# Kernel optimization log

Hardware: AMD Instinct MI355X
Metric: run time of the kernel (lower is better)

Reference implementation:

```python
import jax, jax.numpy as jnp
import numpy as np

N_NODES = 100000
N_EDGES = 1600000
N_GRAPHS = 1024


def gcn_conv(x, src, dst, W, b, num_nodes):
    # GCNConv: x' = D^{-1/2} (A + I) D^{-1/2} x W + b  (self-loops already appended to src/dst)
    h = x @ W  # [N, out]
    deg = jax.ops.segment_sum(jnp.ones_like(dst, dtype=h.dtype), dst, num_segments=num_nodes)
    dinv = jnp.where(deg > 0, jax.lax.rsqrt(jnp.maximum(deg, 1.0)), 0.0)
    norm = dinv[src] * dinv[dst]  # [E]
    msg = h[src] * norm[:, None]  # [E, out]  <- dominant memory traffic
    return jax.ops.segment_sum(msg, dst, num_segments=num_nodes) + b


def global_mean_pool(x, batch, num_graphs):
    s = jax.ops.segment_sum(x, batch, num_segments=num_graphs)
    cnt = jax.ops.segment_sum(jnp.ones((x.shape[0],), x.dtype), batch, num_segments=num_graphs)
    return s / jnp.maximum(cnt, 1.0)[:, None]


def setup_inputs() -> dict:
    key = jax.random.key(0)
    ks = jax.random.split(key, 12)
    x = jax.random.normal(ks[0], (N_NODES, 4), dtype=jnp.float32)
    edge_index = jax.random.randint(ks[1], (2, N_EDGES), 0, N_NODES, dtype=jnp.int64)
    batch = jnp.sort(jax.random.randint(ks[2], (N_NODES,), 0, N_GRAPHS, dtype=jnp.int64))
    def glorot(k, shape):
        fan = shape[0] + shape[1]
        return jax.random.normal(k, shape, jnp.float32) * jnp.sqrt(2.0 / fan)
    return {
        "x": x, "edge_index": edge_index, "batch": batch,
        "W1": glorot(ks[3], (4, 64)),   "b1": jnp.zeros((64,), jnp.float32),
        "W2": glorot(ks[4], (64, 128)), "b2": jnp.zeros((128,), jnp.float32),
        "fc1_W": glorot(ks[5], (128, 64)), "fc1_b": jnp.zeros((64,), jnp.float32),
        "fc2_W": glorot(ks[6], (64, 1)),   "fc2_b": jnp.zeros((1,), jnp.float32),
    }


def reference(x, edge_index, batch, W1, b1, W2, b2, fc1_W, fc1_b, fc2_W, fc2_b):
    n = x.shape[0]
    loops = jnp.arange(n, dtype=edge_index.dtype)
    src = jnp.concatenate([edge_index[0], loops])
    dst = jnp.concatenate([edge_index[1], loops])
    h = jax.nn.relu(gcn_conv(x, src, dst, W1, b1, n))
    h = jax.nn.relu(gcn_conv(h, src, dst, W2, b2, n))
    g = global_mean_pool(h, batch, N_GRAPHS)  # [G, 128]
    g = jax.nn.relu(g @ fc1_W + fc1_b)
    return g @ fc2_W + fc2_b  # [G, 1]
```

## Files before the change

kernel.cpp:

```cpp
#include <hip/hip_runtime.h>
#include <math.h>


#define EPB 8192
#define BSH 8
#define NBUK_MAX 512

__global__ void k_bukhist(const int* __restrict__ dst, int E,
                          int* __restrict__ bkcnt, int nbuk) {
  __shared__ int hist[NBUK_MAX];
  for (int i = threadIdx.x; i < nbuk; i += blockDim.x) hist[i] = 0;
  __syncthreads();
  int i0 = blockIdx.x * EPB, i1 = min(i0 + EPB, E);
  for (int i = i0 + threadIdx.x; i < i1; i += blockDim.x)
    atomicAdd(&hist[dst[i] >> BSH], 1);
  __syncthreads();
  for (int i = threadIdx.x; i < nbuk; i += blockDim.x)
    if (hist[i]) atomicAdd(&bkcnt[i], hist[i]);
}

__global__ void k_scan_buk(const int* __restrict__ bkcnt, int* __restrict__ bcur,
                           int nbuk) {
  __shared__ int sh[NBUK_MAX];
  int t = threadIdx.x;
  int v = (t < nbuk) ? bkcnt[t] : 0;
  sh[t] = v;
  __syncthreads();
  for (int o = 1; o < NBUK_MAX; o <<= 1) {
    int u = (t >= o) ? sh[t - o] : 0;
    __syncthreads();
    sh[t] += u;
    __syncthreads();
  }
  if (t < nbuk) bcur[t] = sh[t] - v;
}

__global__ void k_bucket(const int* __restrict__ src, const int* __restrict__ dst,
                         int E, int* __restrict__ bcur, int* __restrict__ ebuf,
                         int nbuk) {
  __shared__ int hist[NBUK_MAX];
  __shared__ int hbase[NBUK_MAX];
  int t = threadIdx.x;
  int i0 = blockIdx.x * EPB, i1 = min(i0 + EPB, E);
  for (int i = t; i < nbuk; i += blockDim.x) hist[i] = 0;
  __syncthreads();
  for (int i = i0 + t; i < i1; i += blockDim.x)
    atomicAdd(&hist[dst[i] >> BSH], 1);
  __syncthreads();
  for (int i = t; i < nbuk; i += blockDim.x) {
    int c = hist[i];
    hbase[i] = c ? atomicAdd(&bcur[i], c) : 0;
  }
  __syncthreads();
  for (int i = t; i < nbuk; i += blockDim.x) hist[i] = 0;
  __syncthreads();
  for (int i = i0 + t; i < i1; i += blockDim.x) {
    int d = dst[i];
    int b = d >> BSH;
    int pos = hbase[b] + atomicAdd(&hist[b], 1);
    ebuf[pos] = src[i] | ((d & 255) << 17);
  }
}

__global__ void __launch_bounds__(256) k_sortfill(
    const int* __restrict__ ebuf, const int* __restrict__ bcur,
    int* __restrict__ row_ptr, int* __restrict__ csr_src, int N, int nbuk) {
  __shared__ int hist[256];
  __shared__ int sc[256];
  __shared__ int cur[256];
  int b = blockIdx.x, t = threadIdx.x;
  int e0 = (b == 0) ? 0 : bcur[b - 1];
  int e1 = bcur[b];
  hist[t] = 0;
  __syncthreads();
  for (int i = e0 + t; i < e1; i += 256)
    atomicAdd(&hist[ebuf[i] >> 17], 1);
  __syncthreads();
  int v = hist[t];
  sc[t] = v;
  __syncthreads();
  for (int o = 1; o < 256; o <<= 1) {
    int u = (t >= o) ? sc[t - o] : 0;
    __syncthreads();
    sc[t] += u;
    __syncthreads();
  }
  int excl = sc[t] - v;
  int node = (b << BSH) + t;
  if (node < N) row_ptr[node] = e0 + excl;
  if (b == nbuk - 1 && t == 0) row_ptr[N] = e1;
  cur[t] = excl;
  __syncthreads();
  for (int i = e0 + t; i < e1; i += 256) {
    int e = ebuf[i];
    int pos = e0 + atomicAdd(&cur[e >> 17], 1);
    csr_src[pos] = e & 0x1FFFF;
  }
}

__global__ void k_prep(const int* __restrict__ row_ptr, const float* __restrict__ x,
                       float* __restrict__ dinv, float* __restrict__ xp, int N) {
  int i = blockIdx.x * blockDim.x + threadIdx.x;
  if (i < N) {
    int deg = row_ptr[i + 1] - row_ptr[i];
    float di = 1.0f / sqrtf((float)(deg + 1));
    dinv[i] = di;
    float4 v = ((const float4*)x)[i];
    v.x *= di; v.y *= di; v.z *= di; v.w *= di;
    ((float4*)xp)[i] = v;
  }
}

__global__ void k_conv1(const float* __restrict__ xp, const int* __restrict__ row_ptr,
                        const int* __restrict__ csr_src, const float* __restrict__ dinv,
                        const float* __restrict__ W1, const float* __restrict__ b1,
                        float* __restrict__ h1p, int N) {
  int lane = threadIdx.x & 63;
  int sub = lane >> 4, sl = lane & 15;
  int wid = (blockIdx.x * blockDim.x + threadIdx.x) >> 6;
  int nw = (gridDim.x * blockDim.x) >> 6;
  const float4* x4 = (const float4*)xp;
  float w1 = W1[lane], w2 = W1[64 + lane], w3 = W1[128 + lane], w4 = W1[192 + lane];
  float bb = b1[lane];
  for (int base = wid * 4; base < N; base += nw * 4) {
    int n = base + sub;
    bool valid = (n < N);
    int e0 = 0, e1 = 0;
    if (valid) { e0 = row_ptr[n]; e1 = row_ptr[n + 1]; }
    float ax = 0.f, ay = 0.f, az = 0.f, aw = 0.f;
    for (int j = e0 + sl; j < e1; j += 16) {
      float4 xs = x4[csr_src[j]];
      ax += xs.x; ay += xs.y; az += xs.z; aw += xs.w;
    }
#pragma unroll
    for (int o = 8; o; o >>= 1) {
      ax += __shfl_xor(ax, o); ay += __shfl_xor(ay, o);
      az += __shfl_xor(az, o); aw += __shfl_xor(aw, o);
    }
    float di = 0.f;
    if (valid) {
      di = dinv[n];
      float4 xn = x4[n];
      ax += xn.x; ay += xn.y; az += xn.z; aw += xn.w;
    }
#pragma unroll
    for (int g = 0; g < 4; ++g) {
      int nn = base + g;
      if (nn < N) {
        int srcl = g * 16;
        float bx = __shfl(ax, srcl), by = __shfl(ay, srcl);
        float bz = __shfl(az, srcl), bw = __shfl(aw, srcl);
        float dg = __shfl(di, srcl);
        float o0 = bb;
        o0 = fmaf(bx * dg, w1, o0);
        o0 = fmaf(by * dg, w2, o0);
        o0 = fmaf(bz * dg, w3, o0);
        o0 = fmaf(bw * dg, w4, o0);
        h1p[(size_t)nn * 64 + lane] = fmaxf(o0, 0.f) * dg;
      }
    }
  }
}

__global__ void __launch_bounds__(256) k_agg2(
    const float* __restrict__ h1p, const int* __restrict__ row_ptr,
    const int* __restrict__ csr_src, const float* __restrict__ dinv,
    float* __restrict__ agg, int N) {
  int lane = threadIdx.x & 63;
  int wid = (blockIdx.x * blockDim.x + threadIdx.x) >> 6;
  int nw = (gridDim.x * blockDim.x) >> 6;
  for (int n = wid; n < N; n += nw) {
    int e0 = row_ptr[n], e1 = row_ptr[n + 1];
    float a0 = 0.f, a1 = 0.f, a2 = 0.f, a3 = 0.f;
    float a4 = 0.f, a5 = 0.f, a6 = 0.f, a7 = 0.f;
    int j = e0;
    for (; j + 8 <= e1; j += 8) {
      int s0 = csr_src[j + 0], s1 = csr_src[j + 1];
      int s2 = csr_src[j + 2], s3 = csr_src[j + 3];
      int s4 = csr_src[j + 4], s5 = csr_src[j + 5];
      int s6 = csr_src[j + 6], s7 = csr_src[j + 7];
      a0 += h1p[(size_t)s0 * 64 + lane]; a1 += h1p[(size_t)s1 * 64 + lane];
      a2 += h1p[(size_t)s2 * 64 + lane]; a3 += h1p[(size_t)s3 * 64 + lane];
      a4 += h1p[(size_t)s4 * 64 + lane]; a5 += h1p[(size_t)s5 * 64 + lane];
      a6 += h1p[(size_t)s6 * 64 + lane]; a7 += h1p[(size_t)s7 * 64 + lane];
    }
    for (; j + 2 <= e1; j += 2) {
      int s0 = csr_src[j], s1 = csr_src[j + 1];
      a0 += h1p[(size_t)s0 * 64 + lane]; a1 += h1p[(size_t)s1 * 64 + lane];
    }
    if (j < e1) a0 += h1p[(size_t)csr_src[j] * 64 + lane];
    float acc = ((a0 + a1) + (a2 + a3)) + ((a4 + a5) + (a6 + a7));
    acc += h1p[(size_t)n * 64 + lane];
    agg[(size_t)n * 64 + lane] = acc * dinv[n];
  }
}

__global__ void __launch_bounds__(256, 4) k_mm2pool(
    const float* __restrict__ agg, const int* __restrict__ batch,
    const float* __restrict__ W2, const float* __restrict__ b2,
    float* __restrict__ gsum, int N) {
  __shared__ float aT[64][36];
  __shared__ int gid_s[32];
  int tid = threadIdx.x;
  int base = blockIdx.x * 32;
  const float4* agg4 = (const float4*)agg;
  for (int idx = tid; idx < 32 * 16; idx += 256) {
    int node = idx >> 4, chunk = idx & 15;
    int n = base + node;
    float4 v = make_float4(0.f, 0.f, 0.f, 0.f);
    if (n < N) v = agg4[(size_t)n * 16 + chunk];
    aT[chunk * 4 + 0][node] = v.x;
    aT[chunk * 4 + 1][node] = v.y;
    aT[chunk * 4 + 2][node] = v.z;
    aT[chunk * 4 + 3][node] = v.w;
  }
  if (tid < 32) {
    int n = base + tid;
    gid_s[tid] = (n < N) ? batch[n] : -1;
  }
  __syncthreads();
  int c = tid & 127;
  int g = tid >> 7;
  float acc[16];
#pragma unroll
  for (int i = 0; i < 16; ++i) acc[i] = 0.f;
#pragma unroll 4
  for (int k = 0; k < 64; ++k) {
    float w = W2[k * 128 + c];
    const float4* ap = (const float4*)&aT[k][g * 16];
    float4 v0 = ap[0], v1 = ap[1], v2 = ap[2], v3 = ap[3];
    acc[0] = fmaf(v0.x, w, acc[0]);  acc[1] = fmaf(v0.y, w, acc[1]);
    acc[2] = fmaf(v0.z, w, acc[2]);  acc[3] = fmaf(v0.w, w, acc[3]);
    acc[4] = fmaf(v1.x, w, acc[4]);  acc[5] = fmaf(v1.y, w, acc[5]);
    acc[6] = fmaf(v1.z, w, acc[6]);  acc[7] = fmaf(v1.w, w, acc[7]);
    acc[8] = fmaf(v2.x, w, acc[8]);  acc[9] = fmaf(v2.y, w, acc[9]);
    acc[10] = fmaf(v2.z, w, acc[10]); acc[11] = fmaf(v2.w, w, acc[11]);
    acc[12] = fmaf(v3.x, w, acc[12]); acc[13] = fmaf(v3.y, w, acc[13]);
    acc[14] = fmaf(v3.z, w, acc[14]); acc[15] = fmaf(v3.w, w, acc[15]);
  }
  float bias = b2[c];
  float run = 0.f;
  int cur = -1;
#pragma unroll
  for (int i = 0; i < 16; ++i) {
    int n = base + g * 16 + i;
    if (n < N) {
      int gg = gid_s[g * 16 + i];
      float v = fmaxf(acc[i] + bias, 0.f);
      if (gg == cur) {
        run += v;
      } else {
        if (cur >= 0) atomicAdd(&gsum[(size_t)cur * 128 + c], run);
        cur = gg;
        run = v;
      }
    }
  }
  if (cur >= 0) atomicAdd(&gsum[(size_t)cur * 128 + c], run);
}

__device__ __forceinline__ int lower_bound(const int* __restrict__ a, int n, int key) {
  int lo = 0, hi = n;
  while (lo < hi) {
    int m = (lo + hi) >> 1;
    if (a[m] < key) lo = m + 1; else hi = m;
  }
  return lo;
}

__global__ void k_fc(const float* __restrict__ gsum, const int* __restrict__ batch,
                     const float* __restrict__ fc1W, const float* __restrict__ fc1b,
                     const float* __restrict__ fc2W, const float* __restrict__ fc2b,
                     float* __restrict__ out, int N, int G) {
  int g = blockIdx.x;
  int tid = threadIdx.x;
  __shared__ int bnd[2];
  if (tid == 0) bnd[0] = lower_bound(batch, N, g);
  if (tid == 1) bnd[1] = lower_bound(batch, N, g + 1);
  __shared__ float grow[128];
  __syncthreads();
  int cnt = bnd[1] - bnd[0];
  float inv = 1.0f / (float)max(cnt, 1);
  grow[tid] = gsum[(size_t)g * 128 + tid] * inv;
  __syncthreads();
  if (tid < 64) {
    float o = fc1b[tid];
#pragma unroll 8
    for (int k = 0; k < 128; ++k) o = fmaf(grow[k], fc1W[k * 64 + tid], o);
    o = fmaxf(o, 0.f);
    float v = o * fc2W[tid];
#pragma unroll
    for (int off = 32; off; off >>= 1) v += __shfl_xor(v, off);
    if (tid == 0) out[g] = v + fc2b[0];
  }
}

extern "C" void kernel_launch(void* const* d_in, const int* in_sizes, int n_in,
                              void* d_out, int out_size, void* d_ws, size_t ws_size,
                              hipStream_t stream) {
  const float* x = (const float*)d_in[0];
  const int* ei = (const int*)d_in[1];
  const int* batch = (const int*)d_in[2];
  const float* W1 = (const float*)d_in[3];
  const float* b1 = (const float*)d_in[4];
  const float* W2 = (const float*)d_in[5];
  const float* b2 = (const float*)d_in[6];
  const float* fc1W = (const float*)d_in[7];
  const float* fc1b = (const float*)d_in[8];
  const float* fc2W = (const float*)d_in[9];
  const float* fc2b = (const float*)d_in[10];
  float* out = (float*)d_out;

  int N = in_sizes[0] / 4;
  int E = in_sizes[1] / 2;
  int G = out_size;
  const int* src = ei;
  const int* dst = ei + E;

  char* ws = (char*)d_ws;
  size_t off = 0;
  auto take = [&](size_t b) {
    char* p = ws + off;
    off += (b + 255) & ~(size_t)255;
    return p;
  };
  int nbuk = (N + 255) >> BSH;
  int ebl = (E + EPB - 1) / EPB;
  int* row_ptr  = (int*)take((size_t)(N + 1) * 4);
  int* bkcnt    = (int*)take((size_t)NBUK_MAX * 4);
  int* bcur     = (int*)take((size_t)NBUK_MAX * 4);
  float* dinv   = (float*)take((size_t)N * 4);
  float* xp     = (float*)take((size_t)N * 4 * 4);
  int* ebuf     = (int*)take((size_t)E * 4);
  int* csr_src  = (int*)take((size_t)E * 4);
  float* h1p    = (float*)take((size_t)N * 64 * 4);
  float* agg    = (float*)take((size_t)N * 64 * 4);
  float* gsum   = (float*)take((size_t)G * 128 * 4);
  (void)ws_size;

  hipMemsetAsync(bkcnt, 0, (size_t)NBUK_MAX * 4, stream);
  hipMemsetAsync(gsum, 0, (size_t)G * 128 * 4, stream);

  k_bukhist<<<ebl, 256, 0, stream>>>(dst, E, bkcnt, nbuk);
  k_scan_buk<<<1, NBUK_MAX, 0, stream>>>(bkcnt, bcur, nbuk);
  k_bucket<<<ebl, 256, 0, stream>>>(src, dst, E, bcur, ebuf, nbuk);
  k_sortfill<<<nbuk, 256, 0, stream>>>(ebuf, bcur, row_ptr, csr_src, N, nbuk);

  k_prep<<<(N + 255) / 256, 256, 0, stream>>>(row_ptr, x, dinv, xp, N);
  k_conv1<<<2048, 256, 0, stream>>>(xp, row_ptr, csr_src, dinv, W1, b1, h1p, N);
  k_agg2<<<4096, 256, 0, stream>>>(h1p, row_ptr, csr_src, dinv, agg, N);
  k_mm2pool<<<(N + 31) / 32, 256, 0, stream>>>(agg, batch, W2, b2, gsum, N);
  k_fc<<<G, 128, 0, stream>>>(gsum, batch, fc1W, fc1b, fc2W, fc2b, out, N, G);
}
```

Measured before the change: 271.2 us.

## Slice hidden features into 8-channel planes for cache-local gather; fuse prep into sortfill

```diff
diff --git a/kernel.cpp b/kernel.cpp
--- a/kernel.cpp
+++ b/kernel.cpp
@@ -64,7 +64,9 @@
 
 __global__ void __launch_bounds__(256) k_sortfill(
     const int* __restrict__ ebuf, const int* __restrict__ bcur,
-    int* __restrict__ row_ptr, int* __restrict__ csr_src, int N, int nbuk) {
+    const float* __restrict__ x, int* __restrict__ row_ptr,
+    int* __restrict__ csr_src, float* __restrict__ dinv,
+    float* __restrict__ xp, int N, int nbuk) {
   __shared__ int hist[256];
   __shared__ int sc[256];
   __shared__ int cur[256];
@@ -87,7 +89,14 @@
   }
   int excl = sc[t] - v;
   int node = (b << BSH) + t;
-  if (node < N) row_ptr[node] = e0 + excl;
+  if (node < N) {
+    row_ptr[node] = e0 + excl;
+    float di = 1.0f / sqrtf((float)(v + 1));
+    dinv[node] = di;
+    float4 xv = ((const float4*)x)[node];
+    xv.x *= di; xv.y *= di; xv.z *= di; xv.w *= di;
+    ((float4*)xp)[node] = xv;
+  }
   if (b == nbuk - 1 && t == 0) row_ptr[N] = e1;
   cur[t] = excl;
   __syncthreads();
@@ -98,23 +107,10 @@
   }
 }
 
-__global__ void k_prep(const int* __restrict__ row_ptr, const float* __restrict__ x,
-                       float* __restrict__ dinv, float* __restrict__ xp, int N) {
-  int i = blockIdx.x * blockDim.x + threadIdx.x;
-  if (i < N) {
-    int deg = row_ptr[i + 1] - row_ptr[i];
-    float di = 1.0f / sqrtf((float)(deg + 1));
-    dinv[i] = di;
-    float4 v = ((const float4*)x)[i];
-    v.x *= di; v.y *= di; v.z *= di; v.w *= di;
-    ((float4*)xp)[i] = v;
-  }
-}
-
 __global__ void k_conv1(const float* __restrict__ xp, const int* __restrict__ row_ptr,
                         const int* __restrict__ csr_src, const float* __restrict__ dinv,
                         const float* __restrict__ W1, const float* __restrict__ b1,
-                        float* __restrict__ h1p, int N) {
+                        float* __restrict__ h1ps, int N) {
   int lane = threadIdx.x & 63;
   int sub = lane >> 4, sl = lane & 15;
   int wid = (blockIdx.x * blockDim.x + threadIdx.x) >> 6;
@@ -122,6 +118,7 @@
   const float4* x4 = (const float4*)xp;
   float w1 = W1[lane], w2 = W1[64 + lane], w3 = W1[128 + lane], w4 = W1[192 + lane];
   float bb = b1[lane];
+  size_t slice_off = (size_t)(lane >> 3) * N * 8 + (lane & 7);
   for (int base = wid * 4; base < N; base += nw * 4) {
     int n = base + sub;
     bool valid = (n < N);
@@ -156,63 +153,66 @@
         o0 = fmaf(by * dg, w2, o0);
         o0 = fmaf(bz * dg, w3, o0);
         o0 = fmaf(bw * dg, w4, o0);
-        h1p[(size_t)nn * 64 + lane] = fmaxf(o0, 0.f) * dg;
+        h1ps[slice_off + (size_t)nn * 8] = fmaxf(o0, 0.f) * dg;
       }
     }
   }
 }
 
-__global__ void __launch_bounds__(256) k_agg2(
-    const float* __restrict__ h1p, const int* __restrict__ row_ptr,
+__global__ void __launch_bounds__(256) k_agg2s(
+    const float* __restrict__ h1ps, const int* __restrict__ row_ptr,
     const int* __restrict__ csr_src, const float* __restrict__ dinv,
-    float* __restrict__ agg, int N) {
+    float* __restrict__ aggs, int N) {
+  int s = blockIdx.x & 7;
+  int blk = blockIdx.x >> 3;
+  int nblk = gridDim.x >> 3;
+  const float* __restrict__ hs = h1ps + (size_t)s * N * 8;
+  float* __restrict__ as = aggs + (size_t)s * N * 8;
   int lane = threadIdx.x & 63;
-  int wid = (blockIdx.x * blockDim.x + threadIdx.x) >> 6;
-  int nw = (gridDim.x * blockDim.x) >> 6;
-  for (int n = wid; n < N; n += nw) {
-    int e0 = row_ptr[n], e1 = row_ptr[n + 1];
-    float a0 = 0.f, a1 = 0.f, a2 = 0.f, a3 = 0.f;
-    float a4 = 0.f, a5 = 0.f, a6 = 0.f, a7 = 0.f;
-    int j = e0;
-    for (; j + 8 <= e1; j += 8) {
-      int s0 = csr_src[j + 0], s1 = csr_src[j + 1];
-      int s2 = csr_src[j + 2], s3 = csr_src[j + 3];
-      int s4 = csr_src[j + 4], s5 = csr_src[j + 5];
-      int s6 = csr_src[j + 6], s7 = csr_src[j + 7];
-      a0 += h1p[(size_t)s0 * 64 + lane]; a1 += h1p[(size_t)s1 * 64 + lane];
-      a2 += h1p[(size_t)s2 * 64 + lane]; a3 += h1p[(size_t)s3 * 64 + lane];
-      a4 += h1p[(size_t)s4 * 64 + lane]; a5 += h1p[(size_t)s5 * 64 + lane];
-      a6 += h1p[(size_t)s6 * 64 + lane]; a7 += h1p[(size_t)s7 * 64 + lane];
-    }
-    for (; j + 2 <= e1; j += 2) {
-      int s0 = csr_src[j], s1 = csr_src[j + 1];
-      a0 += h1p[(size_t)s0 * 64 + lane]; a1 += h1p[(size_t)s1 * 64 + lane];
-    }
-    if (j < e1) a0 += h1p[(size_t)csr_src[j] * 64 + lane];
-    float acc = ((a0 + a1) + (a2 + a3)) + ((a4 + a5) + (a6 + a7));
-    acc += h1p[(size_t)n * 64 + lane];
-    agg[(size_t)n * 64 + lane] = acc * dinv[n];
+  int sub = lane >> 3;
+  int c = lane & 7;
+  int wv = threadIdx.x >> 6;
+  for (int base = blk * 32 + wv * 8; base < N; base += nblk * 32) {
+    int n = base + sub;
+    if (n < N) {
+      int e0 = row_ptr[n], e1 = row_ptr[n + 1];
+      float a0 = 0.f, a1 = 0.f, a2 = 0.f, a3 = 0.f;
+      int j = e0;
+      for (; j + 4 <= e1; j += 4) {
+        int s0 = csr_src[j], s1 = csr_src[j + 1];
+        int s2 = csr_src[j + 2], s3 = csr_src[j + 3];
+        a0 += hs[(size_t)s0 * 8 + c]; a1 += hs[(size_t)s1 * 8 + c];
+        a2 += hs[(size_t)s2 * 8 + c]; a3 += hs[(size_t)s3 * 8 + c];
+      }
+      for (; j < e1; ++j) a0 += hs[(size_t)csr_src[j] * 8 + c];
+      float acc = (a0 + a1) + (a2 + a3);
+      acc += hs[(size_t)n * 8 + c];
+      as[(size_t)n * 8 + c] = acc * dinv[n];
+    }
   }
 }
 
 __global__ void __launch_bounds__(256, 4) k_mm2pool(
-    const float* __restrict__ agg, const int* __restrict__ batch,
+    const float* __restrict__ aggs, const int* __restrict__ batch,
     const float* __restrict__ W2, const float* __restrict__ b2,
     float* __restrict__ gsum, int N) {
   __shared__ float aT[64][36];
   __shared__ int gid_s[32];
   int tid = threadIdx.x;
   int base = blockIdx.x * 32;
-  const float4* agg4 = (const float4*)agg;
-  for (int idx = tid; idx < 32 * 16; idx += 256) {
-    int node = idx >> 4, chunk = idx & 15;
+  const float4* a4 = (const float4*)aggs;
+  for (int idx = tid; idx < 512; idx += 256) {
+    int s = idx >> 6;
+    int o = idx & 63;
+    int node = o >> 1, h4 = o & 1;
     int n = base + node;
     float4 v = make_float4(0.f, 0.f, 0.f, 0.f);
-    if (n < N) v = agg4[(size_t)n * 16 + chunk];
-    aT[chunk * 4 + 0][node] = v.x;
-    aT[chunk * 4 + 1][node] = v.y;
-    aT[chunk * 4 + 2][node] = v.z;
-    aT[chunk * 4 + 3][node] = v.w;
+    if (n < N) v = a4[((size_t)s * N + n) * 2 + h4];
+    int ch = s * 8 + h4 * 4;
+    aT[ch + 0][node] = v.x;
+    aT[ch + 1][node] = v.y;
+    aT[ch + 2][node] = v.z;
+    aT[ch + 3][node] = v.w;
   }
   if (tid < 32) {
     int n = base + tid;
@@ -333,8 +333,8 @@
   float* xp     = (float*)take((size_t)N * 4 * 4);
   int* ebuf     = (int*)take((size_t)E * 4);
   int* csr_src  = (int*)take((size_t)E * 4);
-  float* h1p    = (float*)take((size_t)N * 64 * 4);
-  float* agg    = (float*)take((size_t)N * 64 * 4);
+  float* h1ps   = (float*)take((size_t)N * 64 * 4);
+  float* aggs   = (float*)take((size_t)N * 64 * 4);
   float* gsum   = (float*)take((size_t)G * 128 * 4);
   (void)ws_size;
 
@@ -344,11 +344,11 @@
   k_bukhist<<<ebl, 256, 0, stream>>>(dst, E, bkcnt, nbuk);
   k_scan_buk<<<1, NBUK_MAX, 0, stream>>>(bkcnt, bcur, nbuk);
   k_bucket<<<ebl, 256, 0, stream>>>(src, dst, E, bcur, ebuf, nbuk);
-  k_sortfill<<<nbuk, 256, 0, stream>>>(ebuf, bcur, row_ptr, csr_src, N, nbuk);
-
-  k_prep<<<(N + 255) / 256, 256, 0, stream>>>(row_ptr, x, dinv, xp, N);
-  k_conv1<<<2048, 256, 0, stream>>>(xp, row_ptr, csr_src, dinv, W1, b1, h1p, N);
-  k_agg2<<<4096, 256, 0, stream>>>(h1p, row_ptr, csr_src, dinv, agg, N);
-  k_mm2pool<<<(N + 31) / 32, 256, 0, stream>>>(agg, batch, W2, b2, gsum, N);
+  k_sortfill<<<nbuk, 256, 0, stream>>>(ebuf, bcur, x, row_ptr, csr_src, dinv, xp, N, nbuk);
+
+  k_conv1<<<2048, 256, 0, stream>>>(xp, row_ptr, csr_src, dinv, W1, b1, h1ps, N);
+  int aggblk = ((N + 31) / 32) * 8;
+  k_agg2s<<<aggblk, 256, 0, stream>>>(h1ps, row_ptr, csr_src, dinv, aggs, N);
+  k_mm2pool<<<(N + 31) / 32, 256, 0, stream>>>(aggs, batch, W2, b2, gsum, N);
   k_fc<<<G, 128, 0, stream>>>(gsum, batch, fc1W, fc1b, fc2W, fc2b, out, N, G);
 }
```

After: 290.1 us. +7.0%, slower.

## Fuse prep into sortfill, sort CSR neighbours, replace pool atomics with slot buffer

Applied to the files above, without the earlier changes.

```diff
diff --git a/kernel.cpp b/kernel.cpp
--- a/kernel.cpp
+++ b/kernel.cpp
@@ -2,9 +2,11 @@
 #include <math.h>
 
 
-#define EPB 8192
+#define EPB 2048
 #define BSH 8
 #define NBUK_MAX 512
+#define SFCAP 5120
+#define SLOTS 12
 
 __global__ void k_bukhist(const int* __restrict__ dst, int E,
                           int* __restrict__ bkcnt, int nbuk) {
@@ -64,13 +66,18 @@
 
 __global__ void __launch_bounds__(256) k_sortfill(
     const int* __restrict__ ebuf, const int* __restrict__ bcur,
-    int* __restrict__ row_ptr, int* __restrict__ csr_src, int N, int nbuk) {
+    const float* __restrict__ x, int* __restrict__ row_ptr,
+    int* __restrict__ csr_src, float* __restrict__ dinv,
+    float* __restrict__ xp, int N, int nbuk) {
   __shared__ int hist[256];
   __shared__ int sc[256];
   __shared__ int cur[256];
+  __shared__ int buf[SFCAP];
   int b = blockIdx.x, t = threadIdx.x;
   int e0 = (b == 0) ? 0 : bcur[b - 1];
   int e1 = bcur[b];
+  int cnt = e1 - e0;
+  bool inlds = (cnt <= SFCAP);
   hist[t] = 0;
   __syncthreads();
   for (int i = e0 + t; i < e1; i += 256)
@@ -87,28 +94,45 @@
   }
   int excl = sc[t] - v;
   int node = (b << BSH) + t;
-  if (node < N) row_ptr[node] = e0 + excl;
+  if (node < N) {
+    row_ptr[node] = e0 + excl;
+    float di = 1.0f / sqrtf((float)(v + 1));
+    dinv[node] = di;
+    float4 xv = ((const float4*)x)[node];
+    xv.x *= di; xv.y *= di; xv.z *= di; xv.w *= di;
+    ((float4*)xp)[node] = xv;
+  }
   if (b == nbuk - 1 && t == 0) row_ptr[N] = e1;
   cur[t] = excl;
   __syncthreads();
   for (int i = e0 + t; i < e1; i += 256) {
     int e = ebuf[i];
-    int pos = e0 + atomicAdd(&cur[e >> 17], 1);
-    csr_src[pos] = e & 0x1FFFF;
-  }
-}
-
-__global__ void k_prep(const int* __restrict__ row_ptr, const float* __restrict__ x,
-                       float* __restrict__ dinv, float* __restrict__ xp, int N) {
-  int i = blockIdx.x * blockDim.x + threadIdx.x;
-  if (i < N) {
-    int deg = row_ptr[i + 1] - row_ptr[i];
-    float di = 1.0f / sqrtf((float)(deg + 1));
-    dinv[i] = di;
-    float4 v = ((const float4*)x)[i];
-    v.x *= di; v.y *= di; v.z *= di; v.w *= di;
-    ((float4*)xp)[i] = v;
-  }
+    int pos = atomicAdd(&cur[e >> 17], 1);
+    if (inlds) buf[pos] = e & 0x1FFFF;
+    else csr_src[e0 + pos] = e & 0x1FFFF;
+  }
+  __syncthreads();
+  if (node < N && v > 1) {
+    if (inlds) {
+      for (int i = 1; i < v; ++i) {
+        int key = buf[excl + i];
+        int j = i - 1;
+        while (j >= 0 && buf[excl + j] > key) { buf[excl + j + 1] = buf[excl + j]; --j; }
+        buf[excl + j + 1] = key;
+      }
+    } else {
+      int s0 = e0 + excl;
+      for (int i = 1; i < v; ++i) {
+        int key = csr_src[s0 + i];
+        int j = i - 1;
+        while (j >= 0 && csr_src[s0 + j] > key) { csr_src[s0 + j + 1] = csr_src[s0 + j]; --j; }
+        csr_src[s0 + j + 1] = key;
+      }
+    }
+  }
+  __syncthreads();
+  if (inlds)
+    for (int i = t; i < cnt; i += 256) csr_src[e0 + i] = buf[i];
 }
 
 __global__ void k_conv1(const float* __restrict__ xp, const int* __restrict__ row_ptr,
@@ -195,12 +219,23 @@
   }
 }
 
+__device__ __forceinline__ int lower_bound(const int* __restrict__ a, int n, int key) {
+  int lo = 0, hi = n;
+  while (lo < hi) {
+    int m = (lo + hi) >> 1;
+    if (a[m] < key) lo = m + 1; else hi = m;
+  }
+  return lo;
+}
+
 __global__ void __launch_bounds__(256, 4) k_mm2pool(
     const float* __restrict__ agg, const int* __restrict__ batch,
     const float* __restrict__ W2, const float* __restrict__ b2,
-    float* __restrict__ gsum, int N) {
+    float* __restrict__ pbuf, int N) {
   __shared__ float aT[64][36];
   __shared__ int gid_s[32];
+  __shared__ int slot_s[32];
+  __shared__ float xf[128];
   int tid = threadIdx.x;
   int base = blockIdx.x * 32;
   const float4* agg4 = (const float4*)agg;
@@ -216,7 +251,11 @@
   }
   if (tid < 32) {
     int n = base + tid;
-    gid_s[tid] = (n < N) ? batch[n] : -1;
+    int gg = (n < N) ? batch[n] : -1;
+    gid_s[tid] = gg;
+    int sl = 0;
+    if (gg >= 0) sl = blockIdx.x - (lower_bound(batch, N, gg) >> 5);
+    slot_s[tid] = (sl < SLOTS) ? sl : (SLOTS - 1);
   }
   __syncthreads();
   int c = tid & 127;
@@ -226,52 +265,70 @@
   for (int i = 0; i < 16; ++i) acc[i] = 0.f;
 #pragma unroll 4
   for (int k = 0; k < 64; ++k) {
-    float w = W2[k * 128 + c];
+    float wv = W2[k * 128 + c];
     const float4* ap = (const float4*)&aT[k][g * 16];
     float4 v0 = ap[0], v1 = ap[1], v2 = ap[2], v3 = ap[3];
-    acc[0] = fmaf(v0.x, w, acc[0]);  acc[1] = fmaf(v0.y, w, acc[1]);
-    acc[2] = fmaf(v0.z, w, acc[2]);  acc[3] = fmaf(v0.w, w, acc[3]);
-    acc[4] = fmaf(v1.x, w, acc[4]);  acc[5] = fmaf(v1.y, w, acc[5]);
-    acc[6] = fmaf(v1.z, w, acc[6]);  acc[7] = fmaf(v1.w, w, acc[7]);
-    acc[8] = fmaf(v2.x, w, acc[8]);  acc[9] = fmaf(v2.y, w, acc[9]);
-    acc[10] = fmaf(v2.z, w, acc[10]); acc[11] = fmaf(v2.w, w, acc[11]);
-    acc[12] = fmaf(v3.x, w, acc[12]); acc[13] = fmaf(v3.y, w, acc[13]);
-    acc[14] = fmaf(v3.z, w, acc[14]); acc[15] = fmaf(v3.w, w, acc[15]);
+    acc[0] = fmaf(v0.x, wv, acc[0]);  acc[1] = fmaf(v0.y, wv, acc[1]);
+    acc[2] = fmaf(v0.z, wv, acc[2]);  acc[3] = fmaf(v0.w, wv, acc[3]);
+    acc[4] = fmaf(v1.x, wv, acc[4]);  acc[5] = fmaf(v1.y, wv, acc[5]);
+    acc[6] = fmaf(v1.z, wv, acc[6]);  acc[7] = fmaf(v1.w, wv, acc[7]);
+    acc[8] = fmaf(v2.x, wv, acc[8]);  acc[9] = fmaf(v2.y, wv, acc[9]);
+    acc[10] = fmaf(v2.z, wv, acc[10]); acc[11] = fmaf(v2.w, wv, acc[11]);
+    acc[12] = fmaf(v3.x, wv, acc[12]); acc[13] = fmaf(v3.y, wv, acc[13]);
+    acc[14] = fmaf(v3.z, wv, acc[14]); acc[15] = fmaf(v3.w, wv, acc[15]);
   }
   float bias = b2[c];
-  float run = 0.f;
-  int cur = -1;
-#pragma unroll
-  for (int i = 0; i < 16; ++i) {
-    int n = base + g * 16 + i;
-    if (n < N) {
-      int gg = gid_s[g * 16 + i];
+  int bnd = (gid_s[16] >= 0 && gid_s[15] == gid_s[16]) ? gid_s[15] : -1;
+  if (g == 1) {
+    float run = 0.f;
+    int cur = -1, curi = -1;
+    bool first = true;
+    for (int i = 0; i < 16; ++i) {
+      int li = 16 + i;
+      if (base + li >= N) break;
+      int gg = gid_s[li];
       float v = fmaxf(acc[i] + bias, 0.f);
-      if (gg == cur) {
-        run += v;
-      } else {
-        if (cur >= 0) atomicAdd(&gsum[(size_t)cur * 128 + c], run);
-        cur = gg;
-        run = v;
+      if (gg == cur) run += v;
+      else {
+        if (cur >= 0) {
+          if (first && cur == bnd) xf[c] = run;
+          else pbuf[((size_t)cur * SLOTS + slot_s[curi]) * 128 + c] = run;
+          first = false;
+        }
+        cur = gg; curi = li; run = v;
       }
     }
-  }
-  if (cur >= 0) atomicAdd(&gsum[(size_t)cur * 128 + c], run);
-}
-
-__device__ __forceinline__ int lower_bound(const int* __restrict__ a, int n, int key) {
-  int lo = 0, hi = n;
-  while (lo < hi) {
-    int m = (lo + hi) >> 1;
-    if (a[m] < key) lo = m + 1; else hi = m;
-  }
-  return lo;
-}
-
-__global__ void k_fc(const float* __restrict__ gsum, const int* __restrict__ batch,
-                     const float* __restrict__ fc1W, const float* __restrict__ fc1b,
-                     const float* __restrict__ fc2W, const float* __restrict__ fc2b,
-                     float* __restrict__ out, int N, int G) {
+    if (cur >= 0) {
+      if (first && cur == bnd) xf[c] = run;
+      else pbuf[((size_t)cur * SLOTS + slot_s[curi]) * 128 + c] = run;
+    }
+  }
+  __syncthreads();
+  if (g == 0) {
+    float run = 0.f;
+    int cur = -1, curi = -1;
+    for (int i = 0; i < 16; ++i) {
+      if (base + i >= N) break;
+      int gg = gid_s[i];
+      float v = fmaxf(acc[i] + bias, 0.f);
+      if (gg == cur) run += v;
+      else {
+        if (cur >= 0)
+          pbuf[((size_t)cur * SLOTS + slot_s[curi]) * 128 + c] = run;
+        cur = gg; curi = i; run = v;
+      }
+    }
+    if (cur >= 0) {
+      if (cur == bnd) run += xf[c];
+      pbuf[((size_t)cur * SLOTS + slot_s[curi]) * 128 + c] = run;
+    }
+  }
+}
+
+__global__ void k_redfc(const float* __restrict__ pbuf, const int* __restrict__ batch,
+                        const float* __restrict__ fc1W, const float* __restrict__ fc1b,
+                        const float* __restrict__ fc2W, const float* __restrict__ fc2b,
+                        float* __restrict__ out, int N, int G) {
   int g = blockIdx.x;
   int tid = threadIdx.x;
   __shared__ int bnd[2];
@@ -279,9 +336,17 @@
   if (tid == 1) bnd[1] = lower_bound(batch, N, g + 1);
   __shared__ float grow[128];
   __syncthreads();
-  int cnt = bnd[1] - bnd[0];
-  float inv = 1.0f / (float)max(cnt, 1);
-  grow[tid] = gsum[(size_t)g * 128 + tid] * inv;
+  int beg = bnd[0], end = bnd[1];
+  int cnt = end - beg;
+  float s = 0.f;
+  if (cnt > 0) {
+    int t0 = beg >> 5, t1 = (end - 1) >> 5;
+    int ns = t1 - t0 + 1;
+    if (ns > SLOTS) ns = SLOTS;
+    for (int sl = 0; sl < ns; ++sl)
+      s += pbuf[((size_t)g * SLOTS + sl) * 128 + tid];
+  }
+  grow[tid] = s / (float)max(cnt, 1);
   __syncthreads();
   if (tid < 64) {
     float o = fc1b[tid];
@@ -335,20 +400,18 @@
   int* csr_src  = (int*)take((size_t)E * 4);
   float* h1p    = (float*)take((size_t)N * 64 * 4);
   float* agg    = (float*)take((size_t)N * 64 * 4);
-  float* gsum   = (float*)take((size_t)G * 128 * 4);
+  float* pbuf   = (float*)take((size_t)G * SLOTS * 128 * 4);
   (void)ws_size;
 
   hipMemsetAsync(bkcnt, 0, (size_t)NBUK_MAX * 4, stream);
-  hipMemsetAsync(gsum, 0, (size_t)G * 128 * 4, stream);
 
   k_bukhist<<<ebl, 256, 0, stream>>>(dst, E, bkcnt, nbuk);
   k_scan_buk<<<1, NBUK_MAX, 0, stream>>>(bkcnt, bcur, nbuk);
   k_bucket<<<ebl, 256, 0, stream>>>(src, dst, E, bcur, ebuf, nbuk);
-  k_sortfill<<<nbuk, 256, 0, stream>>>(ebuf, bcur, row_ptr, csr_src, N, nbuk);
-
-  k_prep<<<(N + 255) / 256, 256, 0, stream>>>(row_ptr, x, dinv, xp, N);
+  k_sortfill<<<nbuk, 256, 0, stream>>>(ebuf, bcur, x, row_ptr, csr_src, dinv, xp, N, nbuk);
+
   k_conv1<<<2048, 256, 0, stream>>>(xp, row_ptr, csr_src, dinv, W1, b1, h1p, N);
   k_agg2<<<4096, 256, 0, stream>>>(h1p, row_ptr, csr_src, dinv, agg, N);
-  k_mm2pool<<<(N + 31) / 32, 256, 0, stream>>>(agg, batch, W2, b2, gsum, N);
-  k_fc<<<G, 128, 0, stream>>>(gsum, batch, fc1W, fc1b, fc2W, fc2b, out, N, G);
-}
+  k_mm2pool<<<(N + 31) / 32, 256, 0, stream>>>(agg, batch, W2, b2, pbuf, N);
+  k_redfc<<<G, 128, 0, stream>>>(pbuf, batch, fc1W, fc1b, fc2W, fc2b, out, N, G);
+}
```

Result: slower. 320.5 us (+18.2%).
